# Performance work log

Measured on AMD Instinct MI355X. Metric: run time of the kernel, lower is better.

Reference implementation:

```python
import jax, jax.numpy as jnp
import numpy as np

N = 50000       # num_nodes
E = 800000      # num_edges (avg degree 16)
DIN = 128       # input_dim
DOUT = 128      # output_dim
H = 4           # num_heads
HD = DOUT // H  # head_dim = 32


def setup_inputs() -> dict:
    key = jax.random.key(0)
    ks = jax.random.split(key, 9)
    x = jax.random.normal(ks[0], (N, DIN), dtype=jnp.float32)
    edge_index = jax.random.randint(ks[1], (2, E), 0, N, dtype=jnp.int64)
    s = 1.0 / np.sqrt(DIN)
    Wq = jax.random.uniform(ks[2], (DOUT, DIN), jnp.float32, -s, s)
    bq = jax.random.uniform(ks[3], (DOUT,), jnp.float32, -s, s)
    Wk = jax.random.uniform(ks[4], (DOUT, DIN), jnp.float32, -s, s)
    bk = jax.random.uniform(ks[5], (DOUT,), jnp.float32, -s, s)
    Wv = jax.random.uniform(ks[6], (DOUT, DIN), jnp.float32, -s, s)
    bv = jax.random.uniform(ks[7], (DOUT,), jnp.float32, -s, s)
    att = jax.random.normal(ks[8], (H, 2 * HD), dtype=jnp.float32)  # nn.Parameter(randn)
    return {"x": x, "edge_index": edge_index, "Wq": Wq, "bq": bq,
            "Wk": Wk, "bk": bk, "Wv": Wv, "bv": bv, "att": att}


def reference(x, edge_index, Wq, bq, Wk, bk, Wv, bv, att):
    n = x.shape[0]
    q = (x @ Wq.T + bq).reshape(n, H, HD)
    k = (x @ Wk.T + bk).reshape(n, H, HD)
    v = (x @ Wv.T + bv).reshape(n, H, HD)
    row, col = edge_index[0], edge_index[1]

    # scores = leaky_relu(sum(cat([q[row],k[col]]) * att)) computed without concat
    a_q, a_k = att[:, :HD], att[:, HD:]                       # [H,HD] each
    scores = jnp.einsum('ehd,hd->eh', q[row], a_q) \
           + jnp.einsum('ehd,hd->eh', k[col], a_k)            # [E,H]
    scores = jax.nn.leaky_relu(scores, 0.2)

    # segment-softmax over edges grouped by destination node (col), per head
    m = jax.ops.segment_max(scores, col, num_segments=n)      # [N,H]
    m = jnp.where(jnp.isfinite(m), m, 0.0)                    # empty segments -> -inf guard
    e = jnp.exp(scores - m[col])                              # [E,H]
    denom = jax.ops.segment_sum(e, col, num_segments=n)       # [N,H]
    w_edge = e / denom[col]                                   # softmax per dst segment

    # attention_weights[i] = mean over incoming edges of softmax weights; 0 if deg==0
    deg = jax.ops.segment_sum(jnp.ones((col.shape[0],), jnp.float32), col,
                              num_segments=n)                 # [N]
    w_sum = jax.ops.segment_sum(w_edge, col, num_segments=n)  # [N,H]
    attn_w = jnp.where(deg[:, None] > 0, w_sum / jnp.maximum(deg, 1.0)[:, None], 0.0)

    # output[dst] += attn_w[dst] * v[src], summed over edges
    msgs = attn_w[col][:, :, None] * v[row]                   # [E,H,HD]
    out = jax.ops.segment_sum(msgs, col, num_segments=n)      # [N,H,HD]
    return out.reshape(n, DOUT)                               # dropout: eval mode (identity)
```

## Files before the change

### kernel.cpp

```cpp
#include <hip/hip_runtime.h>


#define N_NODES 50000
#define N_EDGES 800000
#define SPAN    96
#define NBUCK   521
#define CAP     2304
#define EPB     2048
#define NCHUNK  391
#define GEMMB   391

#define OFF_SORTED 12800000
#define OFF_CURSOR 17601536

typedef __attribute__((ext_vector_type(8))) short short8;
typedef __attribute__((ext_vector_type(4))) float f32x4;

__device__ __forceinline__ unsigned int pack_bf16_rne(float a, float b) {
    unsigned int ua = __float_as_uint(a), ub = __float_as_uint(b);
    unsigned int ha = (ua + 0x7FFFu + ((ua >> 16) & 1u)) >> 16;
    unsigned int hb = (ub + 0x7FFFu + ((ub >> 16) & 1u)) >> 16;
    return ha | (hb << 16);
}
__device__ __forceinline__ unsigned short bf16_rne(float a) {
    unsigned int ua = __float_as_uint(a);
    return (unsigned short)((ua + 0x7FFFu + ((ua >> 16) & 1u)) >> 16);
}
__device__ __forceinline__ float bflo(unsigned int u) { return __uint_as_float(u << 16); }
__device__ __forceinline__ float bfhi(unsigned int u) { return __uint_as_float(u & 0xFFFF0000u); }

__global__ __launch_bounds__(512) void fused_gemm_scatter(
        const float* __restrict__ x, const float* __restrict__ Wv,
        const float* __restrict__ bv, unsigned int* __restrict__ vh,
        const int* __restrict__ ei, int* __restrict__ Cursor,
        unsigned int* __restrict__ sorted) {
    __shared__ __align__(16) unsigned char smem[128 * 68 * 4];
    __shared__ int s_wide;
    int t = threadIdx.x;

    if (blockIdx.x < GEMMB) {
        unsigned int* wB = (unsigned int*)smem;
        for (int q = t; q < 8192; q += 512) {
            int o = q >> 6, k2 = q & 63;
            float2 wp = ((const float2*)Wv)[q];
            wB[o * 68 + k2] = pack_bf16_rne(wp.x, wp.y);
        }
        __syncthreads();

        int lane = t & 63, w = t >> 6;
        int quad = lane >> 4, lc = lane & 15;
        int n0 = blockIdx.x * 128 + w * 16;

        int arow = n0 + lc;
        int arowc = min(arow, N_NODES - 1);
        const float4* xrow = (const float4*)(x + (size_t)arowc * 128);

        f32x4 acc[8];
        #pragma unroll
        for (int ot = 0; ot < 8; ++ot) acc[ot] = (f32x4){0.f, 0.f, 0.f, 0.f};

        #pragma unroll
        for (int ks = 0; ks < 4; ++ks) {
            float4 f0 = xrow[ks * 8 + quad * 2];
            float4 f1 = xrow[ks * 8 + quad * 2 + 1];
            uint4 a4;
            a4.x = pack_bf16_rne(f0.x, f0.y);
            a4.y = pack_bf16_rne(f0.z, f0.w);
            a4.z = pack_bf16_rne(f1.x, f1.y);
            a4.w = pack_bf16_rne(f1.z, f1.w);
            short8 af = *(const short8*)&a4;
            #pragma unroll
            for (int ot = 0; ot < 8; ++ot) {
                uint4 b4 = *(const uint4*)&wB[(ot * 16 + lc) * 68 + ks * 16 + quad * 4];
                short8 bf = *(const short8*)&b4;
                acc[ot] = __builtin_amdgcn_mfma_f32_16x16x32_bf16(af, bf, acc[ot], 0, 0, 0);
            }
        }

        #pragma unroll
        for (int ot = 0; ot < 8; ++ot) {
            int o = ot * 16 + lc;
            float bb = bv[o];
            #pragma unroll
            for (int r = 0; r < 4; ++r) {
                int node = n0 + quad * 4 + r;
                unsigned short u = bf16_rne(acc[ot][r] + bb);
                unsigned int partner = (unsigned int)__shfl_xor((int)u, 1, 64);
                if ((lane & 1) == 0 && node < N_NODES) {
                    unsigned int pair = (unsigned int)u | (partner << 16);
                    vh[(size_t)node * 64 + (o >> 1)] = pair;
                }
            }
        }
    } else {
        unsigned int* w = (unsigned int*)smem;
        int* h    = (int*)(smem + EPB * 4);
        int* base = (int*)(smem + EPB * 4 + NBUCK * 4);
        for (int j = t; j < NBUCK; j += 512) h[j] = 0;
        if (t < 64) {
            int nz = (ei[2 * t + 1] != 0) ? 1 : 0;
            unsigned long long b = __ballot(nz);
            if (t == 0) s_wide = (b == 0ULL) ? 1 : 0;
        }
        __syncthreads();
        int wide = s_wide;
        int e0 = (blockIdx.x - GEMMB) * EPB;

        #pragma unroll
        for (int k = 0; k < EPB / 512; ++k) {
            int e = e0 + k * 512 + t;
            if (e < N_EDGES) {
                int r, c;
                if (wide) {
                    r = (int)((const uint2*)ei)[e].x;
                    c = (int)((const uint2*)ei)[N_EDGES + e].x;
                } else {
                    r = ei[e];
                    c = ei[N_EDGES + e];
                }
                w[k * 512 + t] = ((unsigned int)c << 16) | (unsigned int)r;
                atomicAdd(&h[c / SPAN], 1);
            } else {
                w[k * 512 + t] = 0xFFFFFFFFu;
            }
        }
        __syncthreads();
        for (int j = t; j < NBUCK; j += 512) {
            int cnt = h[j];
            base[j] = cnt ? atomicAdd(&Cursor[j], cnt) : 0;
            h[j] = 0;
        }
        __syncthreads();
        #pragma unroll
        for (int k = 0; k < EPB / 512; ++k) {
            unsigned int ww = w[k * 512 + t];
            if (ww != 0xFFFFFFFFu) {
                int bin = (int)(ww >> 16) / SPAN;
                int p = base[bin] + atomicAdd(&h[bin], 1);
                if (p < CAP)
                    sorted[(size_t)bin * CAP + p] = ww;
            }
        }
    }
}

__global__ __launch_bounds__(512) void gather_kernel(const unsigned int* __restrict__ vh,
                                                     const unsigned int* __restrict__ sorted,
                                                     const int* __restrict__ Cursor,
                                                     float* __restrict__ out) {
    __shared__ unsigned int ww[CAP];
    __shared__ unsigned short rl[CAP];
    __shared__ int deg[SPAN];
    __shared__ int startc[SPAN];
    __shared__ int curp[SPAN];
    __shared__ int sc_s[128];
    int t = threadIdx.x;
    int b = blockIdx.x;
    int nb0 = b * SPAN;
    int span = min(SPAN, N_NODES - nb0);
    int cnt = min(Cursor[b], CAP);
    if (t < SPAN) deg[t] = 0;
    __syncthreads();

    const unsigned int* run = sorted + (size_t)b * CAP;
    for (int i = t; i < cnt; i += 512) {
        unsigned int v = run[i];
        ww[i] = v;
        atomicAdd(&deg[(int)(v >> 16) - nb0], 1);
    }
    __syncthreads();

    if (t < 128) sc_s[t] = (t < SPAN) ? deg[t] : 0;
    __syncthreads();
    for (int off = 1; off < 128; off <<= 1) {
        int y = (t < 128 && t >= off) ? sc_s[t - off] : 0;
        __syncthreads();
        if (t < 128) sc_s[t] += y;
        __syncthreads();
    }
    if (t < SPAN) { startc[t] = sc_s[t] - deg[t]; curp[t] = 0; }
    __syncthreads();

    for (int i = t; i < cnt; i += 512) {
        unsigned int v = ww[i];
        int ln = (int)(v >> 16) - nb0;
        int p = startc[ln] + atomicAdd(&curp[ln], 1);
        rl[p] = (unsigned short)(v & 0xFFFFu);
    }
    __syncthreads();

    int lane = t & 63, wid = t >> 6;
    int quad = lane >> 4;
    int li = lane & 15;
    const uint4* v4 = (const uint4*)vh;

#define ACC8(p) do { \
        c0 += (double)bflo((p).x); c1 += (double)bfhi((p).x); \
        c2 += (double)bflo((p).y); c3 += (double)bfhi((p).y); \
        c4 += (double)bflo((p).z); c5 += (double)bfhi((p).z); \
        c6 += (double)bflo((p).w); c7 += (double)bfhi((p).w); } while (0)

    for (int ln = wid; ln < span; ln += 8) {
        int s0 = startc[ln], d = deg[ln];
        double c0 = 0., c1 = 0., c2 = 0., c3 = 0.;
        double c4 = 0., c5 = 0., c6 = 0., c7 = 0.;
        int j = 0;
        for (; j + 16 <= d; j += 16) {
            int r0 = rl[s0 + j + quad];
            int r1 = rl[s0 + j + 4 + quad];
            int r2 = rl[s0 + j + 8 + quad];
            int r3 = rl[s0 + j + 12 + quad];
            uint4 p0 = v4[(size_t)r0 * 16 + li];
            uint4 p1 = v4[(size_t)r1 * 16 + li];
            uint4 p2 = v4[(size_t)r2 * 16 + li];
            uint4 p3 = v4[(size_t)r3 * 16 + li];
            ACC8(p0); ACC8(p1); ACC8(p2); ACC8(p3);
        }
        for (; j + 4 <= d; j += 4) {
            int r0 = rl[s0 + j + quad];
            uint4 p0 = v4[(size_t)r0 * 16 + li];
            ACC8(p0);
        }
        int rem = d - j;
        if (quad < rem) {
            int r0 = rl[s0 + j + quad];
            uint4 p0 = v4[(size_t)r0 * 16 + li];
            ACC8(p0);
        }
        c0 += __shfl_xor(c0, 16, 64); c0 += __shfl_xor(c0, 32, 64);
        c1 += __shfl_xor(c1, 16, 64); c1 += __shfl_xor(c1, 32, 64);
        c2 += __shfl_xor(c2, 16, 64); c2 += __shfl_xor(c2, 32, 64);
        c3 += __shfl_xor(c3, 16, 64); c3 += __shfl_xor(c3, 32, 64);
        c4 += __shfl_xor(c4, 16, 64); c4 += __shfl_xor(c4, 32, 64);
        c5 += __shfl_xor(c5, 16, 64); c5 += __shfl_xor(c5, 32, 64);
        c6 += __shfl_xor(c6, 16, 64); c6 += __shfl_xor(c6, 32, 64);
        c7 += __shfl_xor(c7, 16, 64); c7 += __shfl_xor(c7, 32, 64);
        if (quad == 0) {
            double sc = (d > 0) ? 1.0 / (double)d : 0.0;
            float4 ra = {(float)(c0 * sc), (float)(c1 * sc),
                         (float)(c2 * sc), (float)(c3 * sc)};
            float4 rb = {(float)(c4 * sc), (float)(c5 * sc),
                         (float)(c6 * sc), (float)(c7 * sc)};
            ((float4*)out)[(size_t)(nb0 + ln) * 32 + 2 * li]     = ra;
            ((float4*)out)[(size_t)(nb0 + ln) * 32 + 2 * li + 1] = rb;
        }
    }
#undef ACC8
}

extern "C" void kernel_launch(void* const* d_in, const int* in_sizes, int n_in,
                              void* d_out, int out_size, void* d_ws, size_t ws_size,
                              hipStream_t stream) {
    const float* x  = (const float*)d_in[0];
    const int*   ei = (const int*)d_in[1];
    const float* Wv = (const float*)d_in[6];
    const float* bv = (const float*)d_in[7];
    float* out = (float*)d_out;

    char* ws = (char*)d_ws;
    unsigned int* vh     = (unsigned int*)(ws);
    unsigned int* sorted = (unsigned int*)(ws + OFF_SORTED);
    int*          Cursor = (int*)(ws + OFF_CURSOR);

    hipMemsetAsync(Cursor, 0, NBUCK * sizeof(int), stream);
    fused_gemm_scatter<<<GEMMB + NCHUNK, 512, 0, stream>>>(x, Wv, bv, vh,
                                                           ei, Cursor, sorted);
    gather_kernel<<<NBUCK, 512, 0, stream>>>(vh, sorted, Cursor, out);
}
```

Baseline: 151.9 us.

## Split each gather bucket across two blocks and use wavefront shuffle scan

The gather kernel now launches two blocks per destination bucket. Each block handles half of the 96-node span and skips edges outside its half, which doubles block-level parallelism across the GPU. The multi-barrier shared-memory prefix scan is replaced by a single-wavefront __shfl_up scan. The cost is that both blocks load and scan the full bucket edge list, so global reads and LDS work for that phase are duplicated.

```diff
diff --git a/kernel.cpp b/kernel.cpp
--- a/kernel.cpp
+++ b/kernel.cpp
@@ -6,6 +6,7 @@
 #define SPAN    96
 #define NBUCK   521
 #define CAP     2304
+#define HSPAN   48
 #define EPB     2048
 #define NCHUNK  391
 #define GEMMB   391
@@ -150,42 +151,47 @@
                                                      float* __restrict__ out) {
     __shared__ unsigned int ww[CAP];
     __shared__ unsigned short rl[CAP];
-    __shared__ int deg[SPAN];
-    __shared__ int startc[SPAN];
-    __shared__ int curp[SPAN];
-    __shared__ int sc_s[128];
+    __shared__ int deg[HSPAN];
+    __shared__ int startc[HSPAN];
+    __shared__ int curp[HSPAN];
     int t = threadIdx.x;
-    int b = blockIdx.x;
-    int nb0 = b * SPAN;
-    int span = min(SPAN, N_NODES - nb0);
+    int b  = blockIdx.x >> 1;
+    int hb = blockIdx.x & 1;
+    int nb0 = b * SPAN + hb * HSPAN;
+    int span = min(HSPAN, N_NODES - nb0);
+    if (span <= 0) return;
     int cnt = min(Cursor[b], CAP);
-    if (t < SPAN) deg[t] = 0;
+    if (t < HSPAN) deg[t] = 0;
     __syncthreads();
 
     const unsigned int* run = sorted + (size_t)b * CAP;
     for (int i = t; i < cnt; i += 512) {
         unsigned int v = run[i];
         ww[i] = v;
-        atomicAdd(&deg[(int)(v >> 16) - nb0], 1);
-    }
-    __syncthreads();
-
-    if (t < 128) sc_s[t] = (t < SPAN) ? deg[t] : 0;
-    __syncthreads();
-    for (int off = 1; off < 128; off <<= 1) {
-        int y = (t < 128 && t >= off) ? sc_s[t - off] : 0;
-        __syncthreads();
-        if (t < 128) sc_s[t] += y;
-        __syncthreads();
-    }
-    if (t < SPAN) { startc[t] = sc_s[t] - deg[t]; curp[t] = 0; }
+        unsigned int ln = (v >> 16) - (unsigned int)nb0;
+        if (ln < (unsigned int)HSPAN) atomicAdd(&deg[ln], 1);
+    }
+    __syncthreads();
+
+    if (t < 64) {
+        int v = (t < HSPAN) ? deg[t] : 0;
+        int s = v;
+        #pragma unroll
+        for (int off = 1; off < 64; off <<= 1) {
+            int y = __shfl_up(s, off, 64);
+            if (t >= off) s += y;
+        }
+        if (t < HSPAN) { startc[t] = s - v; curp[t] = 0; }
+    }
     __syncthreads();
 
     for (int i = t; i < cnt; i += 512) {
         unsigned int v = ww[i];
-        int ln = (int)(v >> 16) - nb0;
-        int p = startc[ln] + atomicAdd(&curp[ln], 1);
-        rl[p] = (unsigned short)(v & 0xFFFFu);
+        unsigned int ln = (v >> 16) - (unsigned int)nb0;
+        if (ln < (unsigned int)HSPAN) {
+            int p = startc[ln] + atomicAdd(&curp[ln], 1);
+            rl[p] = (unsigned short)(v & 0xFFFFu);
+        }
     }
     __syncthreads();
 
@@ -265,5 +271,5 @@
     hipMemsetAsync(Cursor, 0, NBUCK * sizeof(int), stream);
     fused_gemm_scatter<<<GEMMB + NCHUNK, 512, 0, stream>>>(x, Wv, bv, vh,
                                                            ei, Cursor, sorted);
-    gather_kernel<<<NBUCK, 512, 0, stream>>>(vh, sorted, Cursor, out);
-}
+    gather_kernel<<<NBUCK * 2, 512, 0, stream>>>(vh, sorted, Cursor, out);
+}
```

Result: faster. 146.6 us (-3.5%).
